# Kernel optimization log

Measured on AMD Instinct MI355X. Metric: run time of the kernel, lower is better.

Reference implementation:

```python
import jax, jax.numpy as jnp
import numpy as np
from jax import lax

SPLINE_ORDER = 3  # default in KANLinear


def make_grid(in_features, grid_size, order=SPLINE_ORDER):
    # grid_range = [-1, 1], extended by spline_order knots on each side
    h = 2.0 / grid_size
    g = jnp.arange(-order, grid_size + order + 1, dtype=jnp.float32) * h - 1.0
    return jnp.broadcast_to(g, (in_features, g.shape[0]))  # (in, G)


def b_splines(x, grid, order=SPLINE_ORDER):
    # x: (N, in), grid: (in, G). Cox-de Boor recursion.
    x = x[..., None]  # (N, in, 1)
    bases = ((x >= grid[:, :-1]) & (x < grid[:, 1:])).astype(x.dtype)
    for k in range(1, order + 1):
        bases = ((x - grid[:, : -(k + 1)]) / (grid[:, k:-1] - grid[:, : -(k + 1)]) * bases[..., :-1]
                 + (grid[:, k + 1:] - x) / (grid[:, k + 1:] - grid[:, 1:-k]) * bases[..., 1:])
    return bases  # (N, in, grid_size + order)


def kan_conv(x, base_w, spline_w, scaler, grid_size, kernel, pad):
    # x: (B, C, H, W); base_w: (n_convs, K); spline_w: (n_convs, K, grid_size+order); scaler: (n_convs, K)
    B, C, H, W = x.shape
    kh, kw = kernel
    K = kh * kw
    if K == 1:
        p = x.reshape(-1, 1)  # (B*C*H*W, 1)
        Ho, Wo = H, W
    else:
        # patches: (B, C*K, Ho, Wo), feature dim ordered channel-major then (kh, kw)
        patches = lax.conv_general_dilated_patches(x, (kh, kw), (1, 1), [(pad, pad), (pad, pad)])
        Ho, Wo = patches.shape[2], patches.shape[3]
        p = patches.reshape(B, C, K, Ho, Wo).transpose(0, 1, 3, 4, 2).reshape(-1, K)
    grid = make_grid(K, grid_size)
    bases = b_splines(p, grid)  # (N, K, coef) -- shared across all n_convs kernels
    base = jnp.einsum('ni,ki->nk', jax.nn.silu(p), base_w)
    spl = jnp.einsum('nic,kic->nk', bases, spline_w * scaler[..., None])
    n_convs = base_w.shape[0]
    # channel ordering: each input channel expanded into n_convs outputs (channel-major)
    out = (base + spl).reshape(B, C, Ho, Wo, n_convs).transpose(0, 1, 4, 2, 3)
    return out.reshape(B, C * n_convs, Ho, Wo)


def setup_inputs() -> dict:
    key = jax.random.key(0)
    ks = jax.random.split(key, 12)
    B, C, H, W = 4, 3, 256, 256
    coef3 = 3 + SPLINE_ORDER  # grid_size=3 -> 6 spline coefficients
    coef5 = 5 + SPLINE_ORDER  # grid_size=5 (default, kan_conv6) -> 8
    s9 = 1.0 / np.sqrt(9.0)
    return {
        'x': jax.random.normal(ks[0], (B, C, H, W), jnp.float32),
        'base_w1': jax.random.normal(ks[1], (2, 9), jnp.float32) * s9,
        'spline_w1': jax.random.normal(ks[2], (2, 9, coef3), jnp.float32) * 0.1,
        'scaler1': 1.0 + 0.1 * jax.random.normal(ks[3], (2, 9), jnp.float32),
        'base_w2': jax.random.normal(ks[4], (2, 9), jnp.float32) * s9,
        'spline_w2': jax.random.normal(ks[5], (2, 9, coef3), jnp.float32) * 0.1,
        'scaler2': 1.0 + 0.1 * jax.random.normal(ks[6], (2, 9), jnp.float32),
        'conv_w': jax.random.normal(ks[7], (3, 12, 1, 1), jnp.float32) * (1.0 / np.sqrt(12.0)),
        'conv_b': jax.random.normal(ks[8], (3,), jnp.float32) * 0.01,
        'base_w6': jax.random.normal(ks[9], (1, 1), jnp.float32),
        'spline_w6': jax.random.normal(ks[10], (1, 1, coef5), jnp.float32) * 0.1,
        'scaler6': 1.0 + 0.1 * jax.random.normal(ks[11], (1, 1), jnp.float32),
    }


def reference(x, base_w1, spline_w1, scaler1, base_w2, spline_w2, scaler2,
              conv_w, conv_b, base_w6, spline_w6, scaler6):
    x = kan_conv(x, base_w1, spline_w1, scaler1, grid_size=3, kernel=(3, 3), pad=1)   # (B,6,H,W)
    x = kan_conv(x, base_w2, spline_w2, scaler2, grid_size=3, kernel=(3, 3), pad=1)   # (B,12,H,W)
    x = jnp.einsum('bchw,oc->bohw', x, conv_w[:, :, 0, 0]) + conv_b[None, :, None, None]  # 1x1 conv -> (B,3,H,W)
    return kan_conv(x, base_w6, spline_w6, scaler6, grid_size=5, kernel=(1, 1), pad=0)  # (B,3,H,W)
```

## Files before the change

kernel.cpp:

```cpp
#include <hip/hip_runtime.h>
#include <hip/hip_fp16.h>

#define TILE 16

typedef __fp16 h2f __attribute__((ext_vector_type(2)));

union FU { float f; unsigned u; h2f h; };
__device__ __forceinline__ unsigned f2u(float f) { FU t; t.f = f; return t.u; }
__device__ __forceinline__ float    u2f(unsigned u) { FU t; t.u = u; return t.f; }
__device__ __forceinline__ h2f      u2h(unsigned u) { FU t; t.u = u; return t.h; }
__device__ __forceinline__ unsigned h2u(h2f h) { FU t; t.h = h; return t.u; }
__device__ __forceinline__ h2f      f2h(float f) { FU t; t.f = f; return t.h; }

__device__ __forceinline__ float fdot2(h2f a, h2f b, float acc) {
    return __builtin_amdgcn_fdot2(a, b, acc, false);
}

struct Enc { float g, w; unsigned si; };
__device__ __forceinline__ Enc kan_enc3(float v, float g0, float invh, float tmax) {
    Enc e;
    e.g = v / (1.0f + __expf(-v));
    float T = (v - g0) * invh;
    float U = (T >= 0.0f && T < tmax) ? T : -1.0f;
    float mf = floorf(U);
    e.w = U - mf;
    e.si = (unsigned)((int)mf + 1);
    return e;
}

__device__ __forceinline__ float poly_eval(float4 c, float w) {
    return ((c.w * w + c.z) * w + c.y) * w + c.x;
}

__device__ __forceinline__ float4 spline_poly(const float* __restrict__ sw, float sc,
                                              int ncoef, int si) {
    float4 v = make_float4(0.f, 0.f, 0.f, 0.f);
    if (si > 0) {
        int m = si - 1;
        float W[4];
        #pragma unroll
        for (int j = 0; j < 4; ++j) {
            int c = m - 3 + j;
            W[j] = (c >= 0 && c < ncoef) ? sw[c] * sc : 0.0f;
        }
        const float s6 = 1.0f / 6.0f;
        v.x = (W[0] + 4.0f * W[1] + W[2]) * s6;
        v.y = 3.0f * (W[2] - W[0]) * s6;
        v.z = (3.0f * W[0] - 6.0f * W[1] + 3.0f * W[2]) * s6;
        v.w = (W[3] - W[0] + 3.0f * (W[1] - W[2])) * s6;
    }
    return v;
}

__global__ __launch_bounds__(256) void ZS_MKAN_72121090834671_kernel(
    const float* __restrict__ x,
    const float* __restrict__ base_w1, const float* __restrict__ spline_w1,
    const float* __restrict__ scaler1,
    const float* __restrict__ base_w2, const float* __restrict__ spline_w2,
    const float* __restrict__ scaler2,
    const float* __restrict__ conv_w, const float* __restrict__ conv_b,
    const float* __restrict__ base_w6, const float* __restrict__ spline_w6,
    const float* __restrict__ scaler6,
    float* __restrict__ out)
{
    __shared__ float2 encX[1200];
    __shared__ float4 encY[3][324];
    __shared__ uint4  coefH1[9][10];
    __shared__ uint4  coefH2[9][10];
    __shared__ float4 coef6[12];
    __shared__ float  sbw[2][18];
    __shared__ float  scw[36], scb[3];
    __shared__ float  sb6;

    const int tid = threadIdx.x;
    const int tx0 = blockIdx.x * TILE;
    const int ty0 = blockIdx.y * TILE;
    const int b   = blockIdx.z;

    for (int e = tid; e < 180; e += 256) {
        int l = e / 90, r = e % 90, s = r / 10, si = r % 10;
        const float* sw  = l ? spline_w2 : spline_w1;
        const float* scl = l ? scaler2   : scaler1;
        float4 a = spline_poly(sw + s * 6,       scl[s],     6, si);
        float4 c = spline_poly(sw + (9 + s) * 6, scl[9 + s], 6, si);
        uint4 q;
        q.x = h2u(__builtin_amdgcn_cvt_pkrtz(a.x, a.y));
        q.y = h2u(__builtin_amdgcn_cvt_pkrtz(a.z, a.w));
        q.z = h2u(__builtin_amdgcn_cvt_pkrtz(c.x, c.y));
        q.w = h2u(__builtin_amdgcn_cvt_pkrtz(c.z, c.w));
        if (l) coefH2[s][si] = q; else coefH1[s][si] = q;
    }
    if (tid < 12) coef6[tid] = spline_poly(spline_w6, scaler6[0], 8, tid);
    if (tid < 18) { sbw[0][tid] = base_w1[tid]; sbw[1][tid] = base_w2[tid]; }
    if (tid < 36) scw[tid] = conv_w[tid];
    if (tid < 3)  scb[tid] = conv_b[tid];
    if (tid == 0) sb6 = base_w6[0];

    for (int i = tid; i < 1200; i += 256) {
        int c = i / 400, r = i % 400, ly = r / 20, lx = r % 20;
        int gy = ty0 - 2 + ly, gx = tx0 - 2 + lx;
        float v = 0.0f;
        if ((unsigned)gy < 256u && (unsigned)gx < 256u)
            v = x[((b * 3 + c) * 256 + gy) * 256 + gx];
        Enc e = kan_enc3(v, -3.0f, 1.5f, 9.0f);
        unsigned wh = h2u(__builtin_amdgcn_cvt_pkrtz(e.w, 0.0f)) & 0xffffu;
        encX[i] = make_float2(e.g, u2f((e.si << 16) | wh));
    }
    __syncthreads();

    {
        float rb0[9], rb1[9];
        #pragma unroll
        for (int s = 0; s < 9; ++s) { rb0[s] = sbw[0][s]; rb1[s] = sbw[0][9 + s]; }
        for (int i = tid; i < 972; i += 256) {
            int c = i / 324, r = i % 324, ly = r / 18, lx = r % 18;
            float a0 = 0.0f, a1 = 0.0f;
            const float2* ep = &encX[c * 400 + ly * 20 + lx];
            #pragma unroll
            for (int s = 0; s < 9; ++s) {
                float2 e = ep[(s / 3) * 20 + (s % 3)];
                unsigned u = f2u(e.y);
                __fp16 w  = u2h(u).x;
                __fp16 w2 = w * w;
                h2f p1 = {(__fp16)1.0f, w};
                h2f p2 = {w2, (__fp16)(w2 * w)};
                uint4 q = coefH1[s][u >> 16];
                a0 += e.x * rb0[s];
                a1 += e.x * rb1[s];
                a0 = fdot2(u2h(q.x), p1, a0); a0 = fdot2(u2h(q.y), p2, a0);
                a1 = fdot2(u2h(q.z), p1, a1); a1 = fdot2(u2h(q.w), p2, a1);
            }
            int gy = ty0 - 1 + ly, gx = tx0 - 1 + lx;
            if (!((unsigned)gy < 256u && (unsigned)gx < 256u)) { a0 = 0.0f; a1 = 0.0f; }
            Enc e0 = kan_enc3(a0, -3.0f, 1.5f, 9.0f);
            Enc e1 = kan_enc3(a1, -3.0f, 1.5f, 9.0f);
            unsigned w01 = h2u(__builtin_amdgcn_cvt_pkrtz(e0.w, e1.w));
            unsigned s01 = e0.si | (e1.si << 16);
            encY[c][r] = make_float4(e0.g, e1.g, u2f(w01), u2f(s01));
        }
    }
    __syncthreads();

    const int ly = tid >> 4, lx = tid & 15;
    float z[12];
    {
        float rb0[9], rb1[9];
        #pragma unroll
        for (int s = 0; s < 9; ++s) { rb0[s] = sbw[1][s]; rb1[s] = sbw[1][9 + s]; }
        const int rbase = ly * 18 + lx;
        #pragma unroll
        for (int c = 0; c < 3; ++c) {
            float a00 = 0.0f, a01 = 0.0f, a10 = 0.0f, a11 = 0.0f;
            #pragma unroll
            for (int s = 0; s < 9; ++s) {
                float4 e = encY[c][rbase + (s / 3) * 18 + (s % 3)];
                unsigned sv = f2u(e.w);
                h2f wp  = f2h(e.z);
                h2f w2p = wp * wp;
                h2f w3p = w2p * wp;
                h2f p10 = {(__fp16)1.0f, wp.x};
                h2f p20 = {w2p.x, w3p.x};
                h2f p11 = {(__fp16)1.0f, wp.y};
                h2f p21 = {w2p.y, w3p.y};
                uint4 q0 = coefH2[s][sv & 0xffffu];
                uint4 q1 = coefH2[s][sv >> 16];
                a00 += e.x * rb0[s];
                a01 += e.x * rb1[s];
                a10 += e.y * rb0[s];
                a11 += e.y * rb1[s];
                a00 = fdot2(u2h(q0.x), p10, a00); a00 = fdot2(u2h(q0.y), p20, a00);
                a01 = fdot2(u2h(q0.z), p10, a01); a01 = fdot2(u2h(q0.w), p20, a01);
                a10 = fdot2(u2h(q1.x), p11, a10); a10 = fdot2(u2h(q1.y), p21, a10);
                a11 = fdot2(u2h(q1.z), p11, a11); a11 = fdot2(u2h(q1.w), p21, a11);
            }
            z[4 * c + 0] = a00; z[4 * c + 1] = a01;
            z[4 * c + 2] = a10; z[4 * c + 3] = a11;
        }
    }

    const int gy = ty0 + ly, gx = tx0 + lx;
    #pragma unroll
    for (int o = 0; o < 3; ++o) {
        float v = scb[o];
        #pragma unroll
        for (int c = 0; c < 12; ++c) v += scw[o * 12 + c] * z[c];
        Enc t = kan_enc3(v, -2.2f, 2.5f, 11.0f);
        out[((b * 3 + o) * 256 + gy) * 256 + gx] = t.g * sb6 + poly_eval(coef6[t.si], t.w);
    }
}

extern "C" void kernel_launch(void* const* d_in, const int* in_sizes, int n_in,
                              void* d_out, int out_size, void* d_ws, size_t ws_size,
                              hipStream_t stream) {
    (void)in_sizes; (void)n_in; (void)d_ws; (void)ws_size; (void)out_size;
    const float* x         = (const float*)d_in[0];
    const float* base_w1   = (const float*)d_in[1];
    const float* spline_w1 = (const float*)d_in[2];
    const float* scaler1   = (const float*)d_in[3];
    const float* base_w2   = (const float*)d_in[4];
    const float* spline_w2 = (const float*)d_in[5];
    const float* scaler2   = (const float*)d_in[6];
    const float* conv_w    = (const float*)d_in[7];
    const float* conv_b    = (const float*)d_in[8];
    const float* base_w6   = (const float*)d_in[9];
    const float* spline_w6 = (const float*)d_in[10];
    const float* scaler6   = (const float*)d_in[11];
    float* out = (float*)d_out;

    dim3 grid(256 / TILE, 256 / TILE, 4);
    dim3 block(256);
    ZS_MKAN_72121090834671_kernel<<<grid, block, 0, stream>>>(
        x, base_w1, spline_w1, scaler1, base_w2, spline_w2, scaler2,
        conv_w, conv_b, base_w6, spline_w6, scaler6, out);
}
```

Before: 22.30 us.

## Use 16x8 tiles and split layer-2 channels across threads with shared reduction

Halves the tile height to 16x8, so the grid has twice as many blocks. The layer-2 work is now split as three channel groups times 128 pixels across threads, and the partial results are combined through shared memory, which reuses the encX buffer, before 128 threads do the 1x1 conv and the final KAN. The intent is more blocks for better occupancy, with launch_bounds(256,8) added, and an even spread of layer-2 work. The cost is a relatively larger halo recompute per tile (stage-1 covers 10x18 for 8x16 outputs) and an extra barrier, with half the threads idle in the final stage.

```diff
diff --git a/kernel.cpp b/kernel.cpp
--- a/kernel.cpp
+++ b/kernel.cpp
@@ -1,7 +1,8 @@
 #include <hip/hip_runtime.h>
 #include <hip/hip_fp16.h>
 
-#define TILE 16
+#define TW 16
+#define TH 8
 
 typedef __fp16 h2f __attribute__((ext_vector_type(2)));
 
@@ -52,7 +53,7 @@
     return v;
 }
 
-__global__ __launch_bounds__(256) void ZS_MKAN_72121090834671_kernel(
+__global__ __launch_bounds__(256, 8) void ZS_MKAN_72121090834671_kernel(
     const float* __restrict__ x,
     const float* __restrict__ base_w1, const float* __restrict__ spline_w1,
     const float* __restrict__ scaler1,
@@ -63,8 +64,11 @@
     const float* __restrict__ scaler6,
     float* __restrict__ out)
 {
-    __shared__ float2 encX[1200];
-    __shared__ float4 encY[3][324];
+    __shared__ __align__(16) char xz[6656];
+    float2* encX  = (float2*)xz;
+    float*  zpart = (float*)xz;
+
+    __shared__ float4 encY[3][180];
     __shared__ uint4  coefH1[9][10];
     __shared__ uint4  coefH2[9][10];
     __shared__ float4 coef6[12];
@@ -73,12 +77,12 @@
     __shared__ float  sb6;
 
     const int tid = threadIdx.x;
-    const int tx0 = blockIdx.x * TILE;
-    const int ty0 = blockIdx.y * TILE;
+    const int tx0 = blockIdx.x * TW;
+    const int ty0 = blockIdx.y * TH;
     const int b   = blockIdx.z;
 
-    for (int e = tid; e < 180; e += 256) {
-        int l = e / 90, r = e % 90, s = r / 10, si = r % 10;
+    if (tid < 180) {
+        int l = tid / 90, r = tid % 90, s = r / 10, si = r % 10;
         const float* sw  = l ? spline_w2 : spline_w1;
         const float* scl = l ? scaler2   : scaler1;
         float4 a = spline_poly(sw + s * 6,       scl[s],     6, si);
@@ -89,15 +93,19 @@
         q.z = h2u(__builtin_amdgcn_cvt_pkrtz(c.x, c.y));
         q.w = h2u(__builtin_amdgcn_cvt_pkrtz(c.z, c.w));
         if (l) coefH2[s][si] = q; else coefH1[s][si] = q;
-    }
-    if (tid < 12) coef6[tid] = spline_poly(spline_w6, scaler6[0], 8, tid);
-    if (tid < 18) { sbw[0][tid] = base_w1[tid]; sbw[1][tid] = base_w2[tid]; }
-    if (tid < 36) scw[tid] = conv_w[tid];
-    if (tid < 3)  scb[tid] = conv_b[tid];
-    if (tid == 0) sb6 = base_w6[0];
-
-    for (int i = tid; i < 1200; i += 256) {
-        int c = i / 400, r = i % 400, ly = r / 20, lx = r % 20;
+    } else if (tid < 192) {
+        coef6[tid - 180] = spline_poly(spline_w6, scaler6[0], 8, tid - 180);
+    } else if (tid < 228) {
+        int i = tid - 192;
+        scw[i] = conv_w[i];
+        if (i < 18) { sbw[0][i] = base_w1[i]; sbw[1][i] = base_w2[i]; }
+        if (i < 3)  scb[i] = conv_b[i];
+        if (i == 0) sb6 = base_w6[0];
+    }
+    __syncthreads();
+
+    for (int i = tid; i < 720; i += 256) {
+        int c = i / 240, r = i % 240, ly = r / 20, lx = r % 20;
         int gy = ty0 - 2 + ly, gx = tx0 - 2 + lx;
         float v = 0.0f;
         if ((unsigned)gy < 256u && (unsigned)gx < 256u)
@@ -108,84 +116,84 @@
     }
     __syncthreads();
 
-    {
-        float rb0[9], rb1[9];
-        #pragma unroll
-        for (int s = 0; s < 9; ++s) { rb0[s] = sbw[0][s]; rb1[s] = sbw[0][9 + s]; }
-        for (int i = tid; i < 972; i += 256) {
-            int c = i / 324, r = i % 324, ly = r / 18, lx = r % 18;
-            float a0 = 0.0f, a1 = 0.0f;
-            const float2* ep = &encX[c * 400 + ly * 20 + lx];
+    for (int i = tid; i < 540; i += 256) {
+        int c = i / 180, r = i % 180, ly = r / 18, lx = r % 18;
+        float a0 = 0.0f, a1 = 0.0f;
+        const float2* ep = &encX[c * 240 + ly * 20 + lx];
+        #pragma unroll
+        for (int s = 0; s < 9; ++s) {
+            float2 e = ep[(s / 3) * 20 + (s % 3)];
+            unsigned u = f2u(e.y);
+            __fp16 w  = u2h(u).x;
+            __fp16 w2 = w * w;
+            h2f p1 = {(__fp16)1.0f, w};
+            h2f p2 = {w2, (__fp16)(w2 * w)};
+            uint4 q = coefH1[s][u >> 16];
+            a0 += e.x * sbw[0][s];
+            a1 += e.x * sbw[0][9 + s];
+            a0 = fdot2(u2h(q.x), p1, a0); a0 = fdot2(u2h(q.y), p2, a0);
+            a1 = fdot2(u2h(q.z), p1, a1); a1 = fdot2(u2h(q.w), p2, a1);
+        }
+        int gy = ty0 - 1 + ly, gx = tx0 - 1 + lx;
+        if (!((unsigned)gy < 256u && (unsigned)gx < 256u)) { a0 = 0.0f; a1 = 0.0f; }
+        Enc e0 = kan_enc3(a0, -3.0f, 1.5f, 9.0f);
+        Enc e1 = kan_enc3(a1, -3.0f, 1.5f, 9.0f);
+        unsigned w01 = h2u(__builtin_amdgcn_cvt_pkrtz(e0.w, e1.w));
+        unsigned s01 = e0.si | (e1.si << 16);
+        encY[c][r] = make_float4(e0.g, e1.g, u2f(w01), u2f(s01));
+    }
+    __syncthreads();
+
+    for (int u = tid; u < 384; u += 256) {
+        const int pix = u & 127;
+        const int c   = u >> 7;
+        const int ly = pix >> 4, lx = pix & 15;
+        const int rbase = ly * 18 + lx;
+        float a00 = 0.0f, a01 = 0.0f, a10 = 0.0f, a11 = 0.0f;
+        #pragma unroll
+        for (int s = 0; s < 9; ++s) {
+            float4 e = encY[c][rbase + (s / 3) * 18 + (s % 3)];
+            unsigned sv = f2u(e.w);
+            h2f wp  = f2h(e.z);
+            h2f w2p = wp * wp;
+            h2f w3p = w2p * wp;
+            h2f p10 = {(__fp16)1.0f, wp.x};
+            h2f p20 = {w2p.x, w3p.x};
+            h2f p11 = {(__fp16)1.0f, wp.y};
+            h2f p21 = {w2p.y, w3p.y};
+            uint4 q0 = coefH2[s][sv & 0xffffu];
+            uint4 q1 = coefH2[s][sv >> 16];
+            float bw0 = sbw[1][s], bw1 = sbw[1][9 + s];
+            a00 += e.x * bw0;
+            a01 += e.x * bw1;
+            a10 += e.y * bw0;
+            a11 += e.y * bw1;
+            a00 = fdot2(u2h(q0.x), p10, a00); a00 = fdot2(u2h(q0.y), p20, a00);
+            a01 = fdot2(u2h(q0.z), p10, a01); a01 = fdot2(u2h(q0.w), p20, a01);
+            a10 = fdot2(u2h(q1.x), p11, a10); a10 = fdot2(u2h(q1.y), p21, a10);
+            a11 = fdot2(u2h(q1.z), p11, a11); a11 = fdot2(u2h(q1.w), p21, a11);
+        }
+        zpart[pix * 13 + 4 * c + 0] = a00;
+        zpart[pix * 13 + 4 * c + 1] = a01;
+        zpart[pix * 13 + 4 * c + 2] = a10;
+        zpart[pix * 13 + 4 * c + 3] = a11;
+    }
+    __syncthreads();
+
+    if (tid < 128) {
+        const int pix = tid;
+        const int gy = ty0 + (pix >> 4), gx = tx0 + (pix & 15);
+        float z[12];
+        #pragma unroll
+        for (int c = 0; c < 12; ++c) z[c] = zpart[pix * 13 + c];
+        #pragma unroll
+        for (int o = 0; o < 3; ++o) {
+            float v = scb[o];
             #pragma unroll
-            for (int s = 0; s < 9; ++s) {
-                float2 e = ep[(s / 3) * 20 + (s % 3)];
-                unsigned u = f2u(e.y);
-                __fp16 w  = u2h(u).x;
-                __fp16 w2 = w * w;
-                h2f p1 = {(__fp16)1.0f, w};
-                h2f p2 = {w2, (__fp16)(w2 * w)};
-                uint4 q = coefH1[s][u >> 16];
-                a0 += e.x * rb0[s];
-                a1 += e.x * rb1[s];
-                a0 = fdot2(u2h(q.x), p1, a0); a0 = fdot2(u2h(q.y), p2, a0);
-                a1 = fdot2(u2h(q.z), p1, a1); a1 = fdot2(u2h(q.w), p2, a1);
-            }
-            int gy = ty0 - 1 + ly, gx = tx0 - 1 + lx;
-            if (!((unsigned)gy < 256u && (unsigned)gx < 256u)) { a0 = 0.0f; a1 = 0.0f; }
-            Enc e0 = kan_enc3(a0, -3.0f, 1.5f, 9.0f);
-            Enc e1 = kan_enc3(a1, -3.0f, 1.5f, 9.0f);
-            unsigned w01 = h2u(__builtin_amdgcn_cvt_pkrtz(e0.w, e1.w));
-            unsigned s01 = e0.si | (e1.si << 16);
-            encY[c][r] = make_float4(e0.g, e1.g, u2f(w01), u2f(s01));
-        }
-    }
-    __syncthreads();
-
-    const int ly = tid >> 4, lx = tid & 15;
-    float z[12];
-    {
-        float rb0[9], rb1[9];
-        #pragma unroll
-        for (int s = 0; s < 9; ++s) { rb0[s] = sbw[1][s]; rb1[s] = sbw[1][9 + s]; }
-        const int rbase = ly * 18 + lx;
-        #pragma unroll
-        for (int c = 0; c < 3; ++c) {
-            float a00 = 0.0f, a01 = 0.0f, a10 = 0.0f, a11 = 0.0f;
-            #pragma unroll
-            for (int s = 0; s < 9; ++s) {
-                float4 e = encY[c][rbase + (s / 3) * 18 + (s % 3)];
-                unsigned sv = f2u(e.w);
-                h2f wp  = f2h(e.z);
-                h2f w2p = wp * wp;
-                h2f w3p = w2p * wp;
-                h2f p10 = {(__fp16)1.0f, wp.x};
-                h2f p20 = {w2p.x, w3p.x};
-                h2f p11 = {(__fp16)1.0f, wp.y};
-                h2f p21 = {w2p.y, w3p.y};
-                uint4 q0 = coefH2[s][sv & 0xffffu];
-                uint4 q1 = coefH2[s][sv >> 16];
-                a00 += e.x * rb0[s];
-                a01 += e.x * rb1[s];
-                a10 += e.y * rb0[s];
-                a11 += e.y * rb1[s];
-                a00 = fdot2(u2h(q0.x), p10, a00); a00 = fdot2(u2h(q0.y), p20, a00);
-                a01 = fdot2(u2h(q0.z), p10, a01); a01 = fdot2(u2h(q0.w), p20, a01);
-                a10 = fdot2(u2h(q1.x), p11, a10); a10 = fdot2(u2h(q1.y), p21, a10);
-                a11 = fdot2(u2h(q1.z), p11, a11); a11 = fdot2(u2h(q1.w), p21, a11);
-            }
-            z[4 * c + 0] = a00; z[4 * c + 1] = a01;
-            z[4 * c + 2] = a10; z[4 * c + 3] = a11;
-        }
-    }
-
-    const int gy = ty0 + ly, gx = tx0 + lx;
-    #pragma unroll
-    for (int o = 0; o < 3; ++o) {
-        float v = scb[o];
-        #pragma unroll
-        for (int c = 0; c < 12; ++c) v += scw[o * 12 + c] * z[c];
-        Enc t = kan_enc3(v, -2.2f, 2.5f, 11.0f);
-        out[((b * 3 + o) * 256 + gy) * 256 + gx] = t.g * sb6 + poly_eval(coef6[t.si], t.w);
+            for (int c = 0; c < 12; ++c) v += scw[o * 12 + c] * z[c];
+            Enc t = kan_enc3(v, -2.2f, 2.5f, 11.0f);
+            out[((b * 3 + o) * 256 + gy) * 256 + gx] = t.g * sb6 + poly_eval(coef6[t.si], t.w);
+        }
     }
 }
 
@@ -207,7 +215,7 @@
     const float* scaler6   = (const float*)d_in[11];
     float* out = (float*)d_out;
 
-    dim3 grid(256 / TILE, 256 / TILE, 4);
+    dim3 grid(256 / TW, 256 / TH, 4);
     dim3 block(256);
     ZS_MKAN_72121090834671_kernel<<<grid, block, 0, stream>>>(
         x, base_w1, spline_w1, scaler1, base_w2, spline_w2, scaler2,
```

Measured after the change: 23.83 us. 6.8% more time.
